# Kernel optimization log

Hardware: AMD Instinct MI355X
Metric: run time of the kernel (lower is better)

The kernel has to match this reference:

```python
import jax, jax.numpy as jnp
import numpy as np

B, T, D, L = 128, 32, 512, 2


def setup_inputs() -> dict:
    key = jax.random.key(0)
    ks = jax.random.split(key, 8)
    s = 0.02
    inp = {
        "cognition_features": jax.random.normal(ks[0], (B, T, D), dtype=jnp.float32),
        # per-layer stacked params (leading dim L)
        "Wq": s * jax.random.normal(ks[1], (L, D, D), dtype=jnp.float32),
        "bq": jnp.zeros((L, D), jnp.float32),
        "Wk": s * jax.random.normal(ks[2], (L, D, D), dtype=jnp.float32),
        "bk": jnp.zeros((L, D), jnp.float32),
        "Wv": s * jax.random.normal(ks[3], (L, D, D), dtype=jnp.float32),
        "bv": jnp.zeros((L, D), jnp.float32),
        "ln1_g": jnp.ones((L, D), jnp.float32),
        "ln1_b": jnp.zeros((L, D), jnp.float32),
        "W1": s * jax.random.normal(ks[4], (L, 4 * D, D), dtype=jnp.float32),
        "b1": jnp.zeros((L, 4 * D), jnp.float32),
        "W2": s * jax.random.normal(ks[5], (L, D, 4 * D), dtype=jnp.float32),
        "b2": jnp.zeros((L, D), jnp.float32),
        "ln2_g": jnp.ones((L, D), jnp.float32),
        "ln2_b": jnp.zeros((L, D), jnp.float32),
        # gate mlp (random instead of zeros/ones init to avoid degenerate constant gate)
        "Ws": s * jax.random.normal(ks[6], (D, 2 * D), dtype=jnp.float32),
        "bs": jnp.zeros((D,), jnp.float32),
    }
    return inp


def _ln(x, g, b, eps=1e-5):
    mu = jnp.mean(x, axis=-1, keepdims=True)
    var = jnp.mean((x - mu) ** 2, axis=-1, keepdims=True)
    return (x - mu) * jax.lax.rsqrt(var + eps) * g + b


def reference(cognition_features, Wq, bq, Wk, bk, Wv, bv, ln1_g, ln1_b,
              W1, b1, W2, b2, ln2_g, ln2_b, Ws, bs):
    b_, t_, d_ = cognition_features.shape
    L_ = Wq.shape[0]
    # memory bank entries are detached originals of earlier batch items
    mem = jax.lax.stop_gradient(cognition_features).reshape(b_ * t_, d_)
    mem_item = jnp.arange(b_ * t_) // t_
    visible = mem_item[None, :] < jnp.arange(b_)[:, None]  # [B, B*T]
    neg = jnp.asarray(-1e9, cognition_features.dtype)
    scale = 1.0 / jnp.sqrt(jnp.asarray(d_, cognition_features.dtype))

    x = cognition_features
    for l in range(L_):
        q = x @ Wq[l].T + bq[l]                      # [B,T,D]
        k = mem @ Wk[l].T + bk[l]                    # [B*T,D]
        v = mem @ Wv[l].T + bv[l]
        s = jnp.einsum('btd,md->btm', q, k) * scale  # [B,T,B*T]
        s = jnp.where(visible[:, None, :], s, neg)
        a = jax.nn.softmax(s, axis=-1)
        attn = jnp.einsum('btm,md->btd', a, v)
        x = _ln(x + attn, ln1_g[l], ln1_b[l])
        h = jax.nn.gelu(x @ W1[l].T + b1[l], approximate=False)
        x = _ln(x + h @ W2[l].T + b2[l], ln2_g[l], ln2_b[l])

    # item 0 has an empty bank: blocks are skipped, attn_out = query
    attn_out = jnp.where((jnp.arange(b_) == 0)[:, None, None], cognition_features, x)
    cat = jnp.concatenate([cognition_features, attn_out], axis=-1)
    g = jax.nn.sigmoid(cat @ Ws.T + bs)
    return g * cognition_features + (1.0 - g) * attn_out
```

## Files before the change

kernel.cpp:

```cpp
#include <hip/hip_runtime.h>
#include <cmath>


#define ROWS 4096
#define DIM  512

typedef __bf16 bf16x8 __attribute__((ext_vector_type(8)));
typedef float  f32x4  __attribute__((ext_vector_type(4)));
typedef unsigned short u16;
typedef u16 u16x4 __attribute__((ext_vector_type(4)));
typedef u16 u16x8 __attribute__((ext_vector_type(8)));

#define RD ((size_t)ROWS * DIM)
#define BUFU 12288

__device__ __forceinline__ u16 f2bf(float x) {
    union { float f; unsigned u; } c; c.f = x;
    const unsigned r = (c.u + 0x7FFFu + ((c.u >> 16) & 1u)) >> 16;
    return (u16)r;
}

__device__ __forceinline__ void gload16(const void* g, void* l) {
    __builtin_amdgcn_global_load_lds(
        (const __attribute__((address_space(1))) void*)g,
        (__attribute__((address_space(3))) void*)l, 16, 0, 0);
}

__device__ __forceinline__ float gelu_f(float v) {
    return 0.5f * v * (1.0f + erff(v * 0.70710678118654752f));
}

template<int EPI>
__device__ __forceinline__ void mgemm_body(
    const u16* __restrict__ A, int lda,
    const u16* __restrict__ B, int ldb,
    const float* __restrict__ bias,
    void* __restrict__ C, int ldc,
    int kBeg, int kEnd, float scale, int m0, int n0, u16* smem)
{
    const int tid  = threadIdx.x;
    const int lane = tid & 63;
    const int w    = tid >> 6;
    const int wr   = (w >> 1) << 5;
    const int wc   = (w & 1) << 6;

    f32x4 acc[2][4];
    #pragma unroll
    for (int i = 0; i < 2; ++i)
        #pragma unroll
        for (int j = 0; j < 4; ++j)
            acc[i][j] = (f32x4){0.f, 0.f, 0.f, 0.f};

    const u16* gpA[2]; int loA[2];
    #pragma unroll
    for (int q = 0; q < 2; ++q) {
        const int c = (q << 2) + w;
        const int s = (c << 6) + lane;
        const int row = s >> 3, sub = (s & 7) ^ (row & 7);
        gpA[q] = A + (size_t)(m0 + row) * lda + (sub << 3) + kBeg;
        loA[q] = c << 9;
    }
    const u16* gpB[4]; int loB[4];
    #pragma unroll
    for (int q = 0; q < 4; ++q) {
        const int c = ((q + 2) << 2) + w - 8;
        const int s = (c << 6) + lane;
        const int row = s >> 3, sub = (s & 7) ^ (row & 7);
        gpB[q] = B + (size_t)(n0 + row) * ldb + (sub << 3) + kBeg;
        loB[q] = 4096 + (c << 9);
    }

    const int l15 = lane & 15, kg = lane >> 4;
    int aoff[2][2], boff[4][2];
    #pragma unroll
    for (int i = 0; i < 2; ++i)
        #pragma unroll
        for (int h = 0; h < 2; ++h) {
            const int r = wr + (i << 4) + l15;
            const int sub = ((h << 2) + kg) ^ (r & 7);
            aoff[i][h] = ((r << 3) + sub) << 3;
        }
    #pragma unroll
    for (int j = 0; j < 4; ++j)
        #pragma unroll
        for (int h = 0; h < 2; ++h) {
            const int r = wc + (j << 4) + l15;
            const int sub = ((h << 2) + kg) ^ (r & 7);
            boff[j][h] = 4096 + (((r << 3) + sub) << 3);
        }

    const int nt = (kEnd - kBeg) >> 6;

    auto STAGE = [&](int t, int bsel) {
        u16* base = smem + bsel * BUFU;
        const int ko = t << 6;
        gload16(gpA[0] + ko, base + loA[0]);
        gload16(gpA[1] + ko, base + loA[1]);
        gload16(gpB[0] + ko, base + loB[0]);
        gload16(gpB[1] + ko, base + loB[1]);
        gload16(gpB[2] + ko, base + loB[2]);
        gload16(gpB[3] + ko, base + loB[3]);
    };

    if (nt > 0) {
        STAGE(0, 0);
        if (nt > 1) STAGE(1, 1);
        for (int t = 0; t < nt; ++t) {
            if (t + 1 < nt) asm volatile("s_waitcnt vmcnt(6)" ::: "memory");
            else            asm volatile("s_waitcnt vmcnt(0)" ::: "memory");
            __builtin_amdgcn_s_barrier();
            asm volatile("" ::: "memory");

            const u16* buf = smem + (t & 1) * BUFU;
            bf16x8 a_[2][2], b_[4][2];
            #pragma unroll
            for (int i = 0; i < 2; ++i)
                #pragma unroll
                for (int h = 0; h < 2; ++h)
                    a_[i][h] = *reinterpret_cast<const bf16x8*>(&buf[aoff[i][h]]);
            #pragma unroll
            for (int j = 0; j < 4; ++j)
                #pragma unroll
                for (int h = 0; h < 2; ++h)
                    b_[j][h] = *reinterpret_cast<const bf16x8*>(&buf[boff[j][h]]);

            asm volatile("s_waitcnt lgkmcnt(0)" ::: "memory");
            __builtin_amdgcn_s_barrier();
            asm volatile("" ::: "memory");

            if (t + 2 < nt) STAGE(t + 2, t & 1);

            __builtin_amdgcn_s_setprio(1);
            #pragma unroll
            for (int h = 0; h < 2; ++h)
                #pragma unroll
                for (int i = 0; i < 2; ++i)
                    #pragma unroll
                    for (int j = 0; j < 4; ++j) {
                        if (EPI == 4)
                            acc[i][j] = __builtin_amdgcn_mfma_f32_16x16x32_bf16(
                                a_[i][h], b_[j][h], acc[i][j], 0, 0, 0);
                        else
                            acc[i][j] = __builtin_amdgcn_mfma_f32_16x16x32_bf16(
                                b_[j][h], a_[i][h], acc[i][j], 0, 0, 0);
                    }
            __builtin_amdgcn_s_setprio(0);
        }
    }

    const int lq = lane >> 4;
    if (EPI == 4) {
        #pragma unroll
        for (int j = 0; j < 4; ++j) {
            const int col = n0 + wc + (j << 4) + l15;
            const float bj = bias[col];
            #pragma unroll
            for (int i = 0; i < 2; ++i) {
                const int row0 = m0 + wr + (i << 4) + (lq << 2);
                u16x4 pk;
                #pragma unroll
                for (int r = 0; r < 4; ++r) pk[r] = f2bf(acc[i][j][r] + bj);
                *reinterpret_cast<u16x4*>(&((u16*)C)[(size_t)col * ldc + row0]) = pk;
            }
        }
    } else {
        #pragma unroll
        for (int j = 0; j < 4; ++j) {
            const int col0 = n0 + wc + (j << 4) + (lq << 2);
            float4 bj = {0.f, 0.f, 0.f, 0.f};
            if (EPI != 0) bj = *reinterpret_cast<const float4*>(&bias[col0]);
            #pragma unroll
            for (int i = 0; i < 2; ++i) {
                const int row = m0 + wr + (i << 4) + l15;
                f32x4 v = acc[i][j];
                if (EPI == 0) {
                    v[0] *= scale; v[1] *= scale; v[2] *= scale; v[3] *= scale;
                    *reinterpret_cast<f32x4*>(&((float*)C)[(size_t)row * ldc + col0]) = v;
                } else if (EPI == 1) {
                    v[0] += bj.x; v[1] += bj.y; v[2] += bj.z; v[3] += bj.w;
                    *reinterpret_cast<f32x4*>(&((float*)C)[(size_t)row * ldc + col0]) = v;
                } else {
                    v[0] += bj.x; v[1] += bj.y; v[2] += bj.z; v[3] += bj.w;
                    if (EPI == 3) {
                        v[0] = gelu_f(v[0]); v[1] = gelu_f(v[1]);
                        v[2] = gelu_f(v[2]); v[3] = gelu_f(v[3]);
                    }
                    u16x4 pk = {f2bf(v[0]), f2bf(v[1]), f2bf(v[2]), f2bf(v[3])};
                    *reinterpret_cast<u16x4*>(&((u16*)C)[(size_t)row * ldc + col0]) = pk;
                }
            }
        }
    }
}

template<int EPI>
__global__ __launch_bounds__(256, 3) void mgemm(
    const u16* __restrict__ A, int lda, const u16* __restrict__ B, int ldb,
    const float* __restrict__ bias, void* __restrict__ C, int ldc, int K, float scale)
{
    const int m0 = blockIdx.x << 6;
    const int n0 = blockIdx.y << 7;
    __shared__ u16 smem[2 * BUFU];
    mgemm_body<EPI>(A, lda, B, ldb, bias, C, ldc, 0, K, scale, m0, n0, smem);
}

__device__ __forceinline__ int tri_pref(int b) {
    const int h = b >> 1;
    return (b & 1) ? (h + 1) * (h + 1) : h * (h + 1);
}
__global__ __launch_bounds__(256, 3) void mgemm_tri(
    const u16* __restrict__ A, const u16* __restrict__ B,
    float* __restrict__ C, float scale)
{
    const int z = blockIdx.x;
    int bx = 2 * (int)sqrtf((float)z);
    while (tri_pref(bx + 1) <= z) ++bx;
    while (tri_pref(bx) > z) --bx;
    const int by = z - tri_pref(bx);
    __shared__ u16 smem[2 * BUFU];
    mgemm_body<0>(A, 512, B, 512, nullptr, C, 4096, 0, 512, scale,
                  bx << 6, by << 7, smem);
}

template<bool AVK>
__global__ __launch_bounds__(256, 3) void mgemm_pk(
    const u16* __restrict__ A, int lda, const u16* __restrict__ B, int ldb,
    float* __restrict__ Cpart, int K, int chunk)
{
    const int m0 = blockIdx.x << 6;
    const int n0 = blockIdx.y << 7;
    const int z  = blockIdx.z;
    const int Klim = AVK ? (m0 + 64) : K;
    const int ch = AVK ? ((((Klim >> 2) + 63) >> 6) << 6) : chunk;
    int kBeg = z * ch; if (kBeg > Klim) kBeg = Klim;
    int kEnd = kBeg + ch; if (kEnd > Klim) kEnd = Klim;
    __shared__ u16 smem[2 * BUFU];
    mgemm_body<0>(A, lda, B, ldb, nullptr, Cpart + (size_t)z * RD, 512,
                  kBeg, kEnd, 1.f, m0, n0, smem);
}

__global__ __launch_bounds__(256, 3) void qkv_gemm(
    const u16* __restrict__ xa, const u16* __restrict__ cfb,
    const u16* __restrict__ Wqb, const u16* __restrict__ Wkb, const u16* __restrict__ Wvb,
    const float* __restrict__ bq, const float* __restrict__ bk, const float* __restrict__ bv,
    u16* __restrict__ q, u16* __restrict__ k, u16* __restrict__ vT)
{
    __shared__ u16 smem[2 * BUFU];
    const int m0 = blockIdx.x << 6;
    const int which = blockIdx.y >> 2;
    const int n0 = (blockIdx.y & 3) << 7;
    if (which == 0)
        mgemm_body<2>(xa,  512, Wqb, 512, bq, q,  512,  0, 512, 1.f, m0, n0, smem);
    else if (which == 1)
        mgemm_body<2>(cfb, 512, Wkb, 512, bk, k,  512,  0, 512, 1.f, m0, n0, smem);
    else
        mgemm_body<4>(cfb, 512, Wvb, 512, bv, vT, 4096, 0, 512, 1.f, m0, n0, smem);
}

__global__ __launch_bounds__(256) void softmax_pbf(
    const float* __restrict__ S, u16* __restrict__ P, float* __restrict__ sums)
{
    const int row = blockIdx.x;
    const int b   = row >> 5;
    const int Lb  = b << 5;
    const int bound = ((row >> 6) + 1) << 6;
    const float* s = S + (size_t)row * 4096;
    u16* p = P + (size_t)row * 4096;
    const int tid = threadIdx.x;

    const u16x8 z8 = {0, 0, 0, 0, 0, 0, 0, 0};
    for (int m = Lb + tid * 8; m < bound; m += 2048)
        *reinterpret_cast<u16x8*>(&p[m]) = z8;
    if (b == 0) { if (tid == 0) sums[row] = 1.f; return; }

    __shared__ float red[4];
    float mx = -3.0e38f;
    for (int m = tid * 4; m < Lb; m += 1024) {
        const float4 v = *reinterpret_cast<const float4*>(&s[m]);
        mx = fmaxf(mx, fmaxf(fmaxf(v.x, v.y), fmaxf(v.z, v.w)));
    }
    #pragma unroll
    for (int off = 32; off; off >>= 1) mx = fmaxf(mx, __shfl_xor(mx, off));
    if ((tid & 63) == 0) red[tid >> 6] = mx;
    __syncthreads();
    mx = fmaxf(fmaxf(red[0], red[1]), fmaxf(red[2], red[3]));
    __syncthreads();

    float sum = 0.f;
    for (int m = tid * 8; m < Lb; m += 2048) {
        const float4 v0 = *reinterpret_cast<const float4*>(&s[m]);
        const float4 v1 = *reinterpret_cast<const float4*>(&s[m + 4]);
        float e[8];
        e[0] = expf(v0.x - mx); e[1] = expf(v0.y - mx);
        e[2] = expf(v0.z - mx); e[3] = expf(v0.w - mx);
        e[4] = expf(v1.x - mx); e[5] = expf(v1.y - mx);
        e[6] = expf(v1.z - mx); e[7] = expf(v1.w - mx);
        u16x8 o;
        #pragma unroll
        for (int i = 0; i < 8; ++i) { sum += e[i]; o[i] = f2bf(e[i]); }
        *reinterpret_cast<u16x8*>(&p[m]) = o;
    }
    #pragma unroll
    for (int off = 32; off; off >>= 1) sum += __shfl_xor(sum, off);
    if ((tid & 63) == 0) red[tid >> 6] = sum;
    __syncthreads();
    if (tid == 0)
        sums[row] = fmaxf(red[0] + red[1] + red[2] + red[3], 1e-30f);
}

template<int NS, bool HASB, bool DIV>
__global__ __launch_bounds__(256) void ln_res_ps(
    const float* __restrict__ Xin, const float* __restrict__ part,
    const float* __restrict__ bias, const float* __restrict__ sums,
    const float* __restrict__ gamma, const float* __restrict__ beta,
    float* __restrict__ Xout, u16* __restrict__ Xbf)
{
    const int row  = blockIdx.x * 4 + (threadIdx.x >> 6);
    const int lane = threadIdx.x & 63;
    const float* xr = Xin + (size_t)row * DIM;
    const int d0 = lane << 3;
    const float inv = DIV ? (1.0f / sums[row]) : 1.0f;

    const float4 x0 = *reinterpret_cast<const float4*>(&xr[d0]);
    const float4 x1 = *reinterpret_cast<const float4*>(&xr[d0 + 4]);
    float a[8] = {0.f, 0.f, 0.f, 0.f, 0.f, 0.f, 0.f, 0.f};
    #pragma unroll
    for (int s = 0; s < NS; ++s) {
        const float* pr = part + (size_t)s * RD + (size_t)row * DIM + d0;
        const float4 p0 = *reinterpret_cast<const float4*>(pr);
        const float4 p1 = *reinterpret_cast<const float4*>(pr + 4);
        a[0] += p0.x; a[1] += p0.y; a[2] += p0.z; a[3] += p0.w;
        a[4] += p1.x; a[5] += p1.y; a[6] += p1.z; a[7] += p1.w;
    }
    float v[8] = {x0.x, x0.y, x0.z, x0.w, x1.x, x1.y, x1.z, x1.w};
    #pragma unroll
    for (int i = 0; i < 8; ++i) v[i] += a[i] * inv;
    if (HASB) {
        const float4 b0 = *reinterpret_cast<const float4*>(&bias[d0]);
        const float4 b1 = *reinterpret_cast<const float4*>(&bias[d0 + 4]);
        v[0] += b0.x; v[1] += b0.y; v[2] += b0.z; v[3] += b0.w;
        v[4] += b1.x; v[5] += b1.y; v[6] += b1.z; v[7] += b1.w;
    }

    float sm = 0.f;
    #pragma unroll
    for (int i = 0; i < 8; ++i) sm += v[i];
    #pragma unroll
    for (int off = 32; off; off >>= 1) sm += __shfl_xor(sm, off);
    const float mu = sm * (1.0f / 512.0f);

    float qs = 0.f;
    #pragma unroll
    for (int i = 0; i < 8; ++i) { const float d = v[i] - mu; qs += d * d; }
    #pragma unroll
    for (int off = 32; off; off >>= 1) qs += __shfl_xor(qs, off);
    const float rs = rsqrtf(qs * (1.0f / 512.0f) + 1e-5f);

    const float4 g0 = *reinterpret_cast<const float4*>(&gamma[d0]);
    const float4 g1 = *reinterpret_cast<const float4*>(&gamma[d0 + 4]);
    const float4 b0 = *reinterpret_cast<const float4*>(&beta[d0]);
    const float4 b1 = *reinterpret_cast<const float4*>(&beta[d0 + 4]);
    float o[8];
    o[0] = (v[0] - mu) * rs * g0.x + b0.x;
    o[1] = (v[1] - mu) * rs * g0.y + b0.y;
    o[2] = (v[2] - mu) * rs * g0.z + b0.z;
    o[3] = (v[3] - mu) * rs * g0.w + b0.w;
    o[4] = (v[4] - mu) * rs * g1.x + b1.x;
    o[5] = (v[5] - mu) * rs * g1.y + b1.y;
    o[6] = (v[6] - mu) * rs * g1.z + b1.z;
    o[7] = (v[7] - mu) * rs * g1.w + b1.w;

    float4 f0 = {o[0], o[1], o[2], o[3]}, f1 = {o[4], o[5], o[6], o[7]};
    *reinterpret_cast<float4*>(&Xout[(size_t)row * DIM + d0])     = f0;
    *reinterpret_cast<float4*>(&Xout[(size_t)row * DIM + d0 + 4]) = f1;
    u16x8 ob;
    #pragma unroll
    for (int i = 0; i < 8; ++i) ob[i] = f2bf(o[i]);
    *reinterpret_cast<u16x8*>(&Xbf[(size_t)row * DIM + d0]) = ob;
}

struct ConvArgs {
    const float* src[7];
    u16* dst[7];
    int start[8];
};

__global__ __launch_bounds__(256) void conv_all(ConvArgs a)
{
    const int b = blockIdx.x;
    int seg = 0;
    #pragma unroll
    for (int i = 1; i < 7; ++i) seg += (a.start[i] <= b) ? 1 : 0;
    const int i = ((b - a.start[seg]) * 256 + threadIdx.x) << 3;
    const float* s = a.src[seg];
    const float4 lo = *reinterpret_cast<const float4*>(&s[i]);
    const float4 hi = *reinterpret_cast<const float4*>(&s[i + 4]);
    u16x8 o = {f2bf(lo.x), f2bf(lo.y), f2bf(lo.z), f2bf(lo.w),
               f2bf(hi.x), f2bf(hi.y), f2bf(hi.z), f2bf(hi.w)};
    *reinterpret_cast<u16x8*>(&a.dst[seg][i]) = o;
}

__global__ __launch_bounds__(256) void build_cat(
    u16* __restrict__ cat, const u16* __restrict__ cfb, const u16* __restrict__ xbf)
{
    const int idx = blockIdx.x * 256 + threadIdx.x;
    const int row = idx >> 7;
    const int c8  = idx & 127;
    const u16* src2 = (row < 32) ? cfb : xbf;
    const u16x8 v = (c8 < 64)
        ? *reinterpret_cast<const u16x8*>(&cfb[(size_t)row * 512 + (c8 << 3)])
        : *reinterpret_cast<const u16x8*>(&src2[(size_t)row * 512 + ((c8 - 64) << 3)]);
    *reinterpret_cast<u16x8*>(&cat[(size_t)row * 1024 + (c8 << 3)]) = v;
}

__global__ __launch_bounds__(256) void final_gate_ps(
    float4* __restrict__ out, const float4* __restrict__ cf,
    const float4* __restrict__ x, const float* __restrict__ part,
    const float* __restrict__ bias)
{
    const int idx = blockIdx.x * 256 + threadIdx.x;
    const int row = idx >> 7;
    const int c4  = idx & 127;
    const float4 zc = cf[idx];
    const float4 p0 = reinterpret_cast<const float4*>(part)[idx];
    const float4 p1 = reinterpret_cast<const float4*>(part + RD)[idx];
    const float4 bb = *reinterpret_cast<const float4*>(&bias[c4 << 2]);
    const float4 za = (row < 32) ? zc : x[idx];
    float4 o;
    { const float g = 1.0f / (1.0f + expf(-(p0.x + p1.x + bb.x))); o.x = g * zc.x + (1.0f - g) * za.x; }
    { const float g = 1.0f / (1.0f + expf(-(p0.y + p1.y + bb.y))); o.y = g * zc.y + (1.0f - g) * za.y; }
    { const float g = 1.0f / (1.0f + expf(-(p0.z + p1.z + bb.z))); o.z = g * zc.z + (1.0f - g) * za.z; }
    { const float g = 1.0f / (1.0f + expf(-(p0.w + p1.w + bb.w))); o.w = g * zc.w + (1.0f - g) * za.w; }
    out[idx] = o;
}

extern "C" void kernel_launch(void* const* d_in, const int* in_sizes, int n_in,
                              void* d_out, int out_size, void* d_ws, size_t ws_size,
                              hipStream_t stream)
{
    const float* cf   = (const float*)d_in[0];
    const float* Wq   = (const float*)d_in[1];
    const float* bq   = (const float*)d_in[2];
    const float* Wk   = (const float*)d_in[3];
    const float* bk   = (const float*)d_in[4];
    const float* Wv   = (const float*)d_in[5];
    const float* bv   = (const float*)d_in[6];
    const float* ln1g = (const float*)d_in[7];
    const float* ln1b = (const float*)d_in[8];
    const float* W1   = (const float*)d_in[9];
    const float* b1   = (const float*)d_in[10];
    const float* W2   = (const float*)d_in[11];
    const float* b2   = (const float*)d_in[12];
    const float* ln2g = (const float*)d_in[13];
    const float* ln2b = (const float*)d_in[14];
    const float* Wsg  = (const float*)d_in[15];
    const float* bsg  = (const float*)d_in[16];
    float* out = (float*)d_out;

    float* ws   = (float*)d_ws;
    float* x    = ws;
    float* sums = ws + RD;
    float* s    = ws + 2 * RD;
    float* part = ws + 2 * RD;
    u16*  pbf  = (u16*)(ws + 10 * RD);
    u16*  hbf  = pbf;
    u16*  catb = pbf;
    u16*  bfb  = (u16*)(ws + 14 * RD);
    u16* cfb = bfb;
    u16* xbf = bfb + RD;
    u16* qbf = bfb + 2 * RD;
    u16* kbf = bfb + 3 * RD;
    u16* vTb = bfb + 4 * RD;
    u16* Wqb = bfb + 5 * RD;
    u16* Wkb = Wqb + 524288;
    u16* Wvb = Wkb + 524288;
    u16* W1b = Wvb + 524288;
    u16* W2b = W1b + 2097152;
    u16* Wsb = W2b + 2097152;

    const float scale = 0.044194173824159216f;

    ConvArgs ca;
    ca.src[0] = cf;  ca.dst[0] = cfb;
    ca.src[1] = Wq;  ca.dst[1] = Wqb;
    ca.src[2] = Wk;  ca.dst[2] = Wkb;
    ca.src[3] = Wv;  ca.dst[3] = Wvb;
    ca.src[4] = W1;  ca.dst[4] = W1b;
    ca.src[5] = W2;  ca.dst[5] = W2b;
    ca.src[6] = Wsg; ca.dst[6] = Wsb;
    ca.start[0] = 0;    ca.start[1] = 1024; ca.start[2] = 1280;
    ca.start[3] = 1536; ca.start[4] = 1792; ca.start[5] = 2816;
    ca.start[6] = 3840; ca.start[7] = 4096;
    conv_all<<<4096, 256, 0, stream>>>(ca);

    for (int l = 0; l < 2; ++l) {
        const u16* xa = (l == 0) ? cfb : xbf;
        qkv_gemm<<<dim3(64, 12), 256, 0, stream>>>(
            xa, cfb, Wqb + l * 262144, Wkb + l * 262144, Wvb + l * 262144,
            bq + l * 512, bk + l * 512, bv + l * 512, qbf, kbf, vTb);
        mgemm_tri<<<1056, 256, 0, stream>>>(qbf, kbf, s, scale);
        softmax_pbf<<<4096, 256, 0, stream>>>(s, pbf, sums);
        mgemm_pk<true><<<dim3(64, 4, 4), 256, 0, stream>>>(
            pbf, 4096, vTb, 4096, part, 4096, 0);
        ln_res_ps<4, false, true><<<1024, 256, 0, stream>>>(
            (l == 0) ? cf : x, part, nullptr, sums,
            ln1g + l * 512, ln1b + l * 512, x, xbf);
        mgemm<3><<<dim3(64, 16), 256, 0, stream>>>(
            xbf, 512, W1b + l * 1048576, 512, b1 + l * 2048, hbf, 2048, 512, 1.f);
        mgemm_pk<false><<<dim3(64, 4, 4), 256, 0, stream>>>(
            hbf, 2048, W2b + l * 1048576, 2048, part, 2048, 512);
        ln_res_ps<4, true, false><<<1024, 256, 0, stream>>>(
            x, part, b2 + l * 512, nullptr,
            ln2g + l * 512, ln2b + l * 512, x, xbf);
    }

    build_cat<<<2048, 256, 0, stream>>>(catb, cfb, xbf);
    mgemm_pk<false><<<dim3(64, 4, 2), 256, 0, stream>>>(
        catb, 1024, Wsb, 1024, part, 1024, 512);
    final_gate_ps<<<2048, 256, 0, stream>>>((float4*)out, (const float4*)cf,
                                            (const float4*)x, part, bsg);
}
```

Measured before the change: 271.2 us.

## Enlarge GEMM tiles to 128x256 with 8-wave blocks and interleaved staged loads

```diff
diff --git a/kernel.cpp b/kernel.cpp
--- a/kernel.cpp
+++ b/kernel.cpp
@@ -12,7 +12,7 @@
 typedef u16 u16x8 __attribute__((ext_vector_type(8)));
 
 #define RD ((size_t)ROWS * DIM)
-#define BUFU 12288
+#define BUFU 24576
 
 __device__ __forceinline__ u16 f2bf(float x) {
     union { float f; unsigned u; } c; c.f = x;
@@ -31,132 +31,164 @@
 }
 
 template<int EPI>
-__device__ __forceinline__ void mgemm_body(
+__device__ __forceinline__ void mg_body(
     const u16* __restrict__ A, int lda,
     const u16* __restrict__ B, int ldb,
     const float* __restrict__ bias,
     void* __restrict__ C, int ldc,
-    int kBeg, int kEnd, float scale, int m0, int n0, u16* smem)
+    int ktBeg, int ktEnd, float scale, int m0, int n0, u16* smem)
 {
     const int tid  = threadIdx.x;
     const int lane = tid & 63;
-    const int w    = tid >> 6;
-    const int wr   = (w >> 1) << 5;
-    const int wc   = (w & 1) << 6;
-
-    f32x4 acc[2][4];
-    #pragma unroll
-    for (int i = 0; i < 2; ++i)
+    const int wid  = tid >> 6;
+    const int wm   = wid >> 2;
+    const int wn   = wid & 3;
+    const int l15  = lane & 15, kg = lane >> 4, lq = lane >> 4;
+
+    f32x4 acc[4][4];
+    #pragma unroll
+    for (int i = 0; i < 4; ++i)
         #pragma unroll
         for (int j = 0; j < 4; ++j)
             acc[i][j] = (f32x4){0.f, 0.f, 0.f, 0.f};
 
-    const u16* gpA[2]; int loA[2];
-    #pragma unroll
-    for (int q = 0; q < 2; ++q) {
-        const int c = (q << 2) + w;
-        const int s = (c << 6) + lane;
-        const int row = s >> 3, sub = (s & 7) ^ (row & 7);
-        gpA[q] = A + (size_t)(m0 + row) * lda + (sub << 3) + kBeg;
-        loA[q] = c << 9;
-    }
-    const u16* gpB[4]; int loB[4];
-    #pragma unroll
-    for (int q = 0; q < 4; ++q) {
-        const int c = ((q + 2) << 2) + w - 8;
-        const int s = (c << 6) + lane;
-        const int row = s >> 3, sub = (s & 7) ^ (row & 7);
-        gpB[q] = B + (size_t)(n0 + row) * ldb + (sub << 3) + kBeg;
-        loB[q] = 4096 + (c << 9);
-    }
-
-    const int l15 = lane & 15, kg = lane >> 4;
-    int aoff[2][2], boff[4][2];
-    #pragma unroll
-    for (int i = 0; i < 2; ++i)
+    const int sA  = tid,        rA  = sA  >> 2, klA  = (sA  & 3) ^ ((rA  >> 1) & 3);
+    const int sB0 = tid,        rB0 = sB0 >> 2, klB0 = (sB0 & 3) ^ ((rB0 >> 1) & 3);
+    const int sB1 = tid + 512,  rB1 = sB1 >> 2, klB1 = (sB1 & 3) ^ ((rB1 >> 1) & 3);
+    const u16* gA  = A + (size_t)(m0 + rA)  * lda + (klA  << 3) + (size_t)ktBeg * 64;
+    const u16* gB0 = B + (size_t)(n0 + rB0) * ldb + (klB0 << 3) + (size_t)ktBeg * 64;
+    const u16* gB1 = B + (size_t)(n0 + rB1) * ldb + (klB1 << 3) + (size_t)ktBeg * 64;
+    const int dA0 = sA << 3;
+    const int dB0a = 4096  + (sB0 << 3), dB0b = 4096  + (sB1 << 3);
+    const int dA1 = 12288 + (sA << 3);
+    const int dB1a = 16384 + (sB0 << 3), dB1b = 16384 + (sB1 << 3);
+
+    int aoff[2][4], boff[2][4];
+    #pragma unroll
+    for (int ks = 0; ks < 2; ++ks) {
         #pragma unroll
-        for (int h = 0; h < 2; ++h) {
-            const int r = wr + (i << 4) + l15;
-            const int sub = ((h << 2) + kg) ^ (r & 7);
-            aoff[i][h] = ((r << 3) + sub) << 3;
+        for (int ri = 0; ri < 4; ++ri) {
+            const int r = wm * 64 + ri * 16 + l15;
+            aoff[ks][ri] = (ks ? 12288 : 0) + ((r << 2) + (kg ^ ((r >> 1) & 3)) << 3);
         }
-    #pragma unroll
-    for (int j = 0; j < 4; ++j)
         #pragma unroll
-        for (int h = 0; h < 2; ++h) {
-            const int r = wc + (j << 4) + l15;
-            const int sub = ((h << 2) + kg) ^ (r & 7);
-            boff[j][h] = 4096 + (((r << 3) + sub) << 3);
+        for (int cj = 0; cj < 4; ++cj) {
+            const int r = wn * 64 + cj * 16 + l15;
+            boff[ks][cj] = (ks ? 16384 : 4096) + ((r << 2) + (kg ^ ((r >> 1) & 3)) << 3);
         }
-
-    const int nt = (kEnd - kBeg) >> 6;
-
-    auto STAGE = [&](int t, int bsel) {
-        u16* base = smem + bsel * BUFU;
-        const int ko = t << 6;
-        gload16(gpA[0] + ko, base + loA[0]);
-        gload16(gpA[1] + ko, base + loA[1]);
-        gload16(gpB[0] + ko, base + loB[0]);
-        gload16(gpB[1] + ko, base + loB[1]);
-        gload16(gpB[2] + ko, base + loB[2]);
-        gload16(gpB[3] + ko, base + loB[3]);
-    };
+    }
+
+    const int nt = ktEnd - ktBeg;
 
     if (nt > 0) {
-        STAGE(0, 0);
-        if (nt > 1) STAGE(1, 1);
+        {
+            u16* bb = smem;
+            gload16(gA,       bb + dA0);
+            gload16(gB0,      bb + dB0a);
+            gload16(gB1,      bb + dB0b);
+            gload16(gA + 32,  bb + dA1);
+            gload16(gB0 + 32, bb + dB1a);
+            gload16(gB1 + 32, bb + dB1b);
+        }
         for (int t = 0; t < nt; ++t) {
-            if (t + 1 < nt) asm volatile("s_waitcnt vmcnt(6)" ::: "memory");
-            else            asm volatile("s_waitcnt vmcnt(0)" ::: "memory");
+            const u16* bc = smem + (t & 1) * BUFU;
+            u16* bn = smem + ((t + 1) & 1) * BUFU;
+            const bool more = (t + 1 < nt);
+            const int ko = (t + 1) << 6;
+
+            bf16x8 a0, a1, b_[4];
+
+            asm volatile("s_waitcnt vmcnt(3)" ::: "memory");
             __builtin_amdgcn_s_barrier();
             asm volatile("" ::: "memory");
-
-            const u16* buf = smem + (t & 1) * BUFU;
-            bf16x8 a_[2][2], b_[4][2];
-            #pragma unroll
-            for (int i = 0; i < 2; ++i)
-                #pragma unroll
-                for (int h = 0; h < 2; ++h)
-                    a_[i][h] = *reinterpret_cast<const bf16x8*>(&buf[aoff[i][h]]);
+            a0 = *reinterpret_cast<const bf16x8*>(&bc[aoff[0][0]]);
+            a1 = *reinterpret_cast<const bf16x8*>(&bc[aoff[0][1]]);
             #pragma unroll
             for (int j = 0; j < 4; ++j)
-                #pragma unroll
-                for (int h = 0; h < 2; ++h)
-                    b_[j][h] = *reinterpret_cast<const bf16x8*>(&buf[boff[j][h]]);
-
-            asm volatile("s_waitcnt lgkmcnt(0)" ::: "memory");
+                b_[j] = *reinterpret_cast<const bf16x8*>(&bc[boff[0][j]]);
+            if (more) gload16(gA + ko, bn + dA0);
+            __builtin_amdgcn_s_setprio(1);
+            #pragma unroll
+            for (int j = 0; j < 4; ++j) {
+                if (EPI == 4) {
+                    acc[0][j] = __builtin_amdgcn_mfma_f32_16x16x32_bf16(a0, b_[j], acc[0][j], 0, 0, 0);
+                    acc[1][j] = __builtin_amdgcn_mfma_f32_16x16x32_bf16(a1, b_[j], acc[1][j], 0, 0, 0);
+                } else {
+                    acc[0][j] = __builtin_amdgcn_mfma_f32_16x16x32_bf16(b_[j], a0, acc[0][j], 0, 0, 0);
+                    acc[1][j] = __builtin_amdgcn_mfma_f32_16x16x32_bf16(b_[j], a1, acc[1][j], 0, 0, 0);
+                }
+            }
+            __builtin_amdgcn_s_setprio(0);
+
             __builtin_amdgcn_s_barrier();
             asm volatile("" ::: "memory");
-
-            if (t + 2 < nt) STAGE(t + 2, t & 1);
-
+            a0 = *reinterpret_cast<const bf16x8*>(&bc[aoff[0][2]]);
+            a1 = *reinterpret_cast<const bf16x8*>(&bc[aoff[0][3]]);
+            if (more) { gload16(gB0 + ko, bn + dB0a); gload16(gB1 + ko, bn + dB0b); }
             __builtin_amdgcn_s_setprio(1);
             #pragma unroll
-            for (int h = 0; h < 2; ++h)
-                #pragma unroll
-                for (int i = 0; i < 2; ++i)
-                    #pragma unroll
-                    for (int j = 0; j < 4; ++j) {
-                        if (EPI == 4)
-                            acc[i][j] = __builtin_amdgcn_mfma_f32_16x16x32_bf16(
-                                a_[i][h], b_[j][h], acc[i][j], 0, 0, 0);
-                        else
-                            acc[i][j] = __builtin_amdgcn_mfma_f32_16x16x32_bf16(
-                                b_[j][h], a_[i][h], acc[i][j], 0, 0, 0);
-                    }
+            for (int j = 0; j < 4; ++j) {
+                if (EPI == 4) {
+                    acc[2][j] = __builtin_amdgcn_mfma_f32_16x16x32_bf16(a0, b_[j], acc[2][j], 0, 0, 0);
+                    acc[3][j] = __builtin_amdgcn_mfma_f32_16x16x32_bf16(a1, b_[j], acc[3][j], 0, 0, 0);
+                } else {
+                    acc[2][j] = __builtin_amdgcn_mfma_f32_16x16x32_bf16(b_[j], a0, acc[2][j], 0, 0, 0);
+                    acc[3][j] = __builtin_amdgcn_mfma_f32_16x16x32_bf16(b_[j], a1, acc[3][j], 0, 0, 0);
+                }
+            }
+            __builtin_amdgcn_s_setprio(0);
+
+            if (more) asm volatile("s_waitcnt vmcnt(3)" ::: "memory");
+            else      asm volatile("s_waitcnt vmcnt(0)" ::: "memory");
+            __builtin_amdgcn_s_barrier();
+            asm volatile("" ::: "memory");
+            a0 = *reinterpret_cast<const bf16x8*>(&bc[aoff[1][0]]);
+            a1 = *reinterpret_cast<const bf16x8*>(&bc[aoff[1][1]]);
+            #pragma unroll
+            for (int j = 0; j < 4; ++j)
+                b_[j] = *reinterpret_cast<const bf16x8*>(&bc[boff[1][j]]);
+            if (more) gload16(gA + ko + 32, bn + dA1);
+            __builtin_amdgcn_s_setprio(1);
+            #pragma unroll
+            for (int j = 0; j < 4; ++j) {
+                if (EPI == 4) {
+                    acc[0][j] = __builtin_amdgcn_mfma_f32_16x16x32_bf16(a0, b_[j], acc[0][j], 0, 0, 0);
+                    acc[1][j] = __builtin_amdgcn_mfma_f32_16x16x32_bf16(a1, b_[j], acc[1][j], 0, 0, 0);
+                } else {
+                    acc[0][j] = __builtin_amdgcn_mfma_f32_16x16x32_bf16(b_[j], a0, acc[0][j], 0, 0, 0);
+                    acc[1][j] = __builtin_amdgcn_mfma_f32_16x16x32_bf16(b_[j], a1, acc[1][j], 0, 0, 0);
+                }
+            }
+            __builtin_amdgcn_s_setprio(0);
+
+            __builtin_amdgcn_s_barrier();
+            asm volatile("" ::: "memory");
+            a0 = *reinterpret_cast<const bf16x8*>(&bc[aoff[1][2]]);
+            a1 = *reinterpret_cast<const bf16x8*>(&bc[aoff[1][3]]);
+            if (more) { gload16(gB0 + ko + 32, bn + dB1a); gload16(gB1 + ko + 32, bn + dB1b); }
+            __builtin_amdgcn_s_setprio(1);
+            #pragma unroll
+            for (int j = 0; j < 4; ++j) {
+                if (EPI == 4) {
+                    acc[2][j] = __builtin_amdgcn_mfma_f32_16x16x32_bf16(a0, b_[j], acc[2][j], 0, 0, 0);
+                    acc[3][j] = __builtin_amdgcn_mfma_f32_16x16x32_bf16(a1, b_[j], acc[3][j], 0, 0, 0);
+                } else {
+                    acc[2][j] = __builtin_amdgcn_mfma_f32_16x16x32_bf16(b_[j], a0, acc[2][j], 0, 0, 0);
+                    acc[3][j] = __builtin_amdgcn_mfma_f32_16x16x32_bf16(b_[j], a1, acc[3][j], 0, 0, 0);
+                }
+            }
             __builtin_amdgcn_s_setprio(0);
         }
     }
 
-    const int lq = lane >> 4;
     if (EPI == 4) {
         #pragma unroll
         for (int j = 0; j < 4; ++j) {
-            const int col = n0 + wc + (j << 4) + l15;
+            const int col = n0 + wn * 64 + (j << 4) + l15;
             const float bj = bias[col];
             #pragma unroll
-            for (int i = 0; i < 2; ++i) {
-                const int row0 = m0 + wr + (i << 4) + (lq << 2);
+            for (int i = 0; i < 4; ++i) {
+                const int row0 = m0 + wm * 64 + (i << 4) + (lq << 2);
                 u16x4 pk;
                 #pragma unroll
                 for (int r = 0; r < 4; ++r) pk[r] = f2bf(acc[i][j][r] + bj);
@@ -166,18 +198,15 @@
     } else {
         #pragma unroll
         for (int j = 0; j < 4; ++j) {
-            const int col0 = n0 + wc + (j << 4) + (lq << 2);
+            const int col0 = n0 + wn * 64 + (j << 4) + (lq << 2);
             float4 bj = {0.f, 0.f, 0.f, 0.f};
             if (EPI != 0) bj = *reinterpret_cast<const float4*>(&bias[col0]);
             #pragma unroll
-            for (int i = 0; i < 2; ++i) {
-                const int row = m0 + wr + (i << 4) + l15;
+            for (int i = 0; i < 4; ++i) {
+                const int row = m0 + wm * 64 + (i << 4) + l15;
                 f32x4 v = acc[i][j];
                 if (EPI == 0) {
                     v[0] *= scale; v[1] *= scale; v[2] *= scale; v[3] *= scale;
-                    *reinterpret_cast<f32x4*>(&((float*)C)[(size_t)row * ldc + col0]) = v;
-                } else if (EPI == 1) {
-                    v[0] += bj.x; v[1] += bj.y; v[2] += bj.z; v[3] += bj.w;
                     *reinterpret_cast<f32x4*>(&((float*)C)[(size_t)row * ldc + col0]) = v;
                 } else {
                     v[0] += bj.x; v[1] += bj.y; v[2] += bj.z; v[3] += bj.w;
@@ -193,68 +222,84 @@
     }
 }
 
-template<int EPI>
-__global__ __launch_bounds__(256, 3) void mgemm(
-    const u16* __restrict__ A, int lda, const u16* __restrict__ B, int ldb,
-    const float* __restrict__ bias, void* __restrict__ C, int ldc, int K, float scale)
-{
-    const int m0 = blockIdx.x << 6;
-    const int n0 = blockIdx.y << 7;
+__global__ __launch_bounds__(512, 2) void g_qkv(
+    const u16* __restrict__ xa, const u16* __restrict__ cfb,
+    const u16* __restrict__ Wqb, const u16* __restrict__ Wkb,
+    const u16* __restrict__ Wvb,
+    const float* __restrict__ bq, const float* __restrict__ bk,
+    const float* __restrict__ bv,
+    u16* __restrict__ q, u16* __restrict__ k, u16* __restrict__ vT)
+{
     __shared__ u16 smem[2 * BUFU];
-    mgemm_body<EPI>(A, lda, B, ldb, bias, C, ldc, 0, K, scale, m0, n0, smem);
+    const int m0 = blockIdx.x << 7;
+    const int which = blockIdx.y >> 1;
+    const int n0 = (blockIdx.y & 1) << 8;
+    if (which == 0)
+        mg_body<2>(xa,  512, Wqb, 512, bq, q,  512,  0, 8, 1.f, m0, n0, smem);
+    else if (which == 1)
+        mg_body<2>(cfb, 512, Wkb, 512, bk, k,  512,  0, 8, 1.f, m0, n0, smem);
+    else
+        mg_body<4>(cfb, 512, Wvb, 512, bv, vT, 4096, 0, 8, 1.f, m0, n0, smem);
 }
 
 __device__ __forceinline__ int tri_pref(int b) {
     const int h = b >> 1;
     return (b & 1) ? (h + 1) * (h + 1) : h * (h + 1);
 }
-__global__ __launch_bounds__(256, 3) void mgemm_tri(
-    const u16* __restrict__ A, const u16* __restrict__ B,
-    float* __restrict__ C, float scale)
+__global__ __launch_bounds__(512, 2) void g_tri(
+    const u16* __restrict__ qb, const u16* __restrict__ kb,
+    float* __restrict__ S, float scale)
 {
     const int z = blockIdx.x;
-    int bx = 2 * (int)sqrtf((float)z);
-    while (tri_pref(bx + 1) <= z) ++bx;
-    while (tri_pref(bx) > z) --bx;
-    const int by = z - tri_pref(bx);
+    int mt = 2 * (int)sqrtf((float)z);
+    while (tri_pref(mt + 1) <= z) ++mt;
+    while (tri_pref(mt) > z) --mt;
+    const int nt = z - tri_pref(mt);
     __shared__ u16 smem[2 * BUFU];
-    mgemm_body<0>(A, 512, B, 512, nullptr, C, 4096, 0, 512, scale,
-                  bx << 6, by << 7, smem);
-}
-
-template<bool AVK>
-__global__ __launch_bounds__(256, 3) void mgemm_pk(
-    const u16* __restrict__ A, int lda, const u16* __restrict__ B, int ldb,
-    float* __restrict__ Cpart, int K, int chunk)
-{
-    const int m0 = blockIdx.x << 6;
-    const int n0 = blockIdx.y << 7;
-    const int z  = blockIdx.z;
-    const int Klim = AVK ? (m0 + 64) : K;
-    const int ch = AVK ? ((((Klim >> 2) + 63) >> 6) << 6) : chunk;
-    int kBeg = z * ch; if (kBeg > Klim) kBeg = Klim;
-    int kEnd = kBeg + ch; if (kEnd > Klim) kEnd = Klim;
+    mg_body<0>(qb, 512, kb, 512, nullptr, S, 4096, 0, 8, scale, mt << 7, nt << 8, smem);
+}
+
+__global__ __launch_bounds__(512, 2) void g_av(
+    const u16* __restrict__ P, const u16* __restrict__ vT,
+    float* __restrict__ part)
+{
+    const int mt = blockIdx.x, n0 = blockIdx.y << 8, z = blockIdx.z;
+    const int kts = 2 * mt + 2;
+    const int ch = (kts + 3) >> 2;
+    int kb = z * ch; if (kb > kts) kb = kts;
+    int ke = kb + ch; if (ke > kts) ke = kts;
     __shared__ u16 smem[2 * BUFU];
-    mgemm_body<0>(A, lda, B, ldb, nullptr, Cpart + (size_t)z * RD, 512,
-                  kBeg, kEnd, 1.f, m0, n0, smem);
-}
-
-__global__ __launch_bounds__(256, 3) void qkv_gemm(
-    const u16* __restrict__ xa, const u16* __restrict__ cfb,
-    const u16* __restrict__ Wqb, const u16* __restrict__ Wkb, const u16* __restrict__ Wvb,
-    const float* __restrict__ bq, const float* __restrict__ bk, const float* __restrict__ bv,
-    u16* __restrict__ q, u16* __restrict__ k, u16* __restrict__ vT)
+    mg_body<0>(P, 4096, vT, 4096, nullptr, part + (size_t)z * RD, 512,
+               kb, ke, 1.f, mt << 7, n0, smem);
+}
+
+__global__ __launch_bounds__(512, 2) void g_mlp1(
+    const u16* __restrict__ xb, const u16* __restrict__ W1b,
+    const float* __restrict__ b1, u16* __restrict__ h)
 {
     __shared__ u16 smem[2 * BUFU];
-    const int m0 = blockIdx.x << 6;
-    const int which = blockIdx.y >> 2;
-    const int n0 = (blockIdx.y & 3) << 7;
-    if (which == 0)
-        mgemm_body<2>(xa,  512, Wqb, 512, bq, q,  512,  0, 512, 1.f, m0, n0, smem);
-    else if (which == 1)
-        mgemm_body<2>(cfb, 512, Wkb, 512, bk, k,  512,  0, 512, 1.f, m0, n0, smem);
-    else
-        mgemm_body<4>(cfb, 512, Wvb, 512, bv, vT, 4096, 0, 512, 1.f, m0, n0, smem);
+    mg_body<3>(xb, 512, W1b, 512, b1, h, 2048, 0, 8, 1.f,
+               blockIdx.x << 7, blockIdx.y << 8, smem);
+}
+
+__global__ __launch_bounds__(512, 2) void g_mlp2(
+    const u16* __restrict__ h, const u16* __restrict__ W2b,
+    float* __restrict__ part)
+{
+    const int z = blockIdx.z;
+    __shared__ u16 smem[2 * BUFU];
+    mg_body<0>(h, 2048, W2b, 2048, nullptr, part + (size_t)z * RD, 512,
+               z * 8, z * 8 + 8, 1.f, blockIdx.x << 7, blockIdx.y << 8, smem);
+}
+
+__global__ __launch_bounds__(512, 2) void g_gate(
+    const u16* __restrict__ cat, const u16* __restrict__ Wsb,
+    float* __restrict__ part)
+{
+    const int z = blockIdx.z;
+    __shared__ u16 smem[2 * BUFU];
+    mg_body<0>(cat, 1024, Wsb, 1024, nullptr, part + (size_t)z * RD, 512,
+               z * 8, z * 8 + 8, 1.f, blockIdx.x << 7, blockIdx.y << 8, smem);
 }
 
 __global__ __launch_bounds__(256) void softmax_pbf(
@@ -263,7 +308,7 @@
     const int row = blockIdx.x;
     const int b   = row >> 5;
     const int Lb  = b << 5;
-    const int bound = ((row >> 6) + 1) << 6;
+    const int bound = ((row >> 7) + 1) << 7;
     const float* s = S + (size_t)row * 4096;
     u16* p = P + (size_t)row * 4096;
     const int tid = threadIdx.x;
@@ -463,8 +508,8 @@
     float* s    = ws + 2 * RD;
     float* part = ws + 2 * RD;
     u16*  pbf  = (u16*)(ws + 10 * RD);
-    u16*  hbf  = pbf;
-    u16*  catb = pbf;
+    u16*  hbf  = (u16*)(ws + 10 * RD);
+    u16*  catb = (u16*)(ws + 10 * RD);
     u16*  bfb  = (u16*)(ws + 14 * RD);
     u16* cfb = bfb;
     u16* xbf = bfb + RD;
@@ -495,28 +540,25 @@
 
     for (int l = 0; l < 2; ++l) {
         const u16* xa = (l == 0) ? cfb : xbf;
-        qkv_gemm<<<dim3(64, 12), 256, 0, stream>>>(
+        g_qkv<<<dim3(32, 6), 512, 0, stream>>>(
             xa, cfb, Wqb + l * 262144, Wkb + l * 262144, Wvb + l * 262144,
             bq + l * 512, bk + l * 512, bv + l * 512, qbf, kbf, vTb);
-        mgemm_tri<<<1056, 256, 0, stream>>>(qbf, kbf, s, scale);
+        g_tri<<<272, 512, 0, stream>>>(qbf, kbf, s, scale);
         softmax_pbf<<<4096, 256, 0, stream>>>(s, pbf, sums);
-        mgemm_pk<true><<<dim3(64, 4, 4), 256, 0, stream>>>(
-            pbf, 4096, vTb, 4096, part, 4096, 0);
+        g_av<<<dim3(32, 2, 4), 512, 0, stream>>>(pbf, vTb, part);
         ln_res_ps<4, false, true><<<1024, 256, 0, stream>>>(
             (l == 0) ? cf : x, part, nullptr, sums,
             ln1g + l * 512, ln1b + l * 512, x, xbf);
-        mgemm<3><<<dim3(64, 16), 256, 0, stream>>>(
-            xbf, 512, W1b + l * 1048576, 512, b1 + l * 2048, hbf, 2048, 512, 1.f);
-        mgemm_pk<false><<<dim3(64, 4, 4), 256, 0, stream>>>(
-            hbf, 2048, W2b + l * 1048576, 2048, part, 2048, 512);
+        g_mlp1<<<dim3(32, 8), 512, 0, stream>>>(
+            xbf, W1b + l * 1048576, b1 + l * 2048, hbf);
+        g_mlp2<<<dim3(32, 2, 4), 512, 0, stream>>>(hbf, W2b + l * 1048576, part);
         ln_res_ps<4, true, false><<<1024, 256, 0, stream>>>(
             x, part, b2 + l * 512, nullptr,
             ln2g + l * 512, ln2b + l * 512, x, xbf);
     }
 
     build_cat<<<2048, 256, 0, stream>>>(catb, cfb, xbf);
-    mgemm_pk<false><<<dim3(64, 4, 2), 256, 0, stream>>>(
-        catb, 1024, Wsb, 1024, part, 1024, 512);
+    g_gate<<<dim3(32, 2, 2), 512, 0, stream>>>(catb, Wsb, part);
     final_gate_ps<<<2048, 256, 0, stream>>>((float4*)out, (const float4*)cf,
                                             (const float4*)x, part, bsg);
 }
```

After: 307.8 us. 13.5% more time.

## Fuse softmax exponentiation into the QK^T GEMM epilogue and drop the concat copy

Applied to the files above, without the earlier changes.

```diff
diff --git a/kernel.cpp b/kernel.cpp
--- a/kernel.cpp
+++ b/kernel.cpp
@@ -36,7 +36,8 @@
     const u16* __restrict__ B, int ldb,
     const float* __restrict__ bias,
     void* __restrict__ C, int ldc,
-    int kBeg, int kEnd, float scale, int m0, int n0, u16* smem)
+    int kBeg, int kEnd, float scale, int m0, int n0, u16* smem,
+    float* __restrict__ sums)
 {
     const int tid  = threadIdx.x;
     const int lane = tid & 63;
@@ -162,6 +163,34 @@
                 for (int r = 0; r < 4; ++r) pk[r] = f2bf(acc[i][j][r] + bj);
                 *reinterpret_cast<u16x4*>(&((u16*)C)[(size_t)col * ldc + row0]) = pk;
             }
+        }
+    } else if (EPI == 5) {
+        float rs0 = 0.f, rs1 = 0.f;
+        #pragma unroll
+        for (int j = 0; j < 4; ++j) {
+            const int col0 = n0 + wc + (j << 4) + (lq << 2);
+            #pragma unroll
+            for (int i = 0; i < 2; ++i) {
+                const int row = m0 + wr + (i << 4) + l15;
+                const int lim = (row >> 5) << 5;
+                f32x4 v = acc[i][j];
+                u16x4 pk;
+                float rsl = 0.f;
+                #pragma unroll
+                for (int r = 0; r < 4; ++r) {
+                    const float e = (col0 + r < lim) ? __expf(v[r] * scale) : 0.f;
+                    rsl += e;
+                    pk[r] = f2bf(e);
+                }
+                if (i == 0) rs0 += rsl; else rs1 += rsl;
+                *reinterpret_cast<u16x4*>(&((u16*)C)[(size_t)row * ldc + col0]) = pk;
+            }
+        }
+        rs0 += __shfl_xor(rs0, 16); rs0 += __shfl_xor(rs0, 32);
+        rs1 += __shfl_xor(rs1, 16); rs1 += __shfl_xor(rs1, 32);
+        if (lq == 0) {
+            atomicAdd(&sums[m0 + wr + l15], rs0);
+            atomicAdd(&sums[m0 + wr + 16 + l15], rs1);
         }
     } else {
         #pragma unroll
@@ -201,7 +230,7 @@
     const int m0 = blockIdx.x << 6;
     const int n0 = blockIdx.y << 7;
     __shared__ u16 smem[2 * BUFU];
-    mgemm_body<EPI>(A, lda, B, ldb, bias, C, ldc, 0, K, scale, m0, n0, smem);
+    mgemm_body<EPI>(A, lda, B, ldb, bias, C, ldc, 0, K, scale, m0, n0, smem, nullptr);
 }
 
 __device__ __forceinline__ int tri_pref(int b) {
@@ -210,7 +239,7 @@
 }
 __global__ __launch_bounds__(256, 3) void mgemm_tri(
     const u16* __restrict__ A, const u16* __restrict__ B,
-    float* __restrict__ C, float scale)
+    u16* __restrict__ P, float* __restrict__ sums, float scale)
 {
     const int z = blockIdx.x;
     int bx = 2 * (int)sqrtf((float)z);
@@ -218,8 +247,8 @@
     while (tri_pref(bx) > z) --bx;
     const int by = z - tri_pref(bx);
     __shared__ u16 smem[2 * BUFU];
-    mgemm_body<0>(A, 512, B, 512, nullptr, C, 4096, 0, 512, scale,
-                  bx << 6, by << 7, smem);
+    mgemm_body<5>(A, 512, B, 512, nullptr, P, 4096, 0, 512, scale,
+                  bx << 6, by << 7, smem, sums);
 }
 
 template<bool AVK>
@@ -236,7 +265,18 @@
     int kEnd = kBeg + ch; if (kEnd > Klim) kEnd = Klim;
     __shared__ u16 smem[2 * BUFU];
     mgemm_body<0>(A, lda, B, ldb, nullptr, Cpart + (size_t)z * RD, 512,
-                  kBeg, kEnd, 1.f, m0, n0, smem);
+                  kBeg, kEnd, 1.f, m0, n0, smem, nullptr);
+}
+
+__global__ __launch_bounds__(256, 3) void mgemm_part(
+    const u16* __restrict__ A, int lda, const u16* __restrict__ B, int ldb,
+    float* __restrict__ Cpart)
+{
+    const int m0 = blockIdx.x << 6;
+    const int n0 = blockIdx.y << 7;
+    __shared__ u16 smem[2 * BUFU];
+    mgemm_body<0>(A, lda, B, ldb, nullptr, Cpart, 512,
+                  0, 512, 1.f, m0, n0, smem, nullptr);
 }
 
 __global__ __launch_bounds__(256, 3) void qkv_gemm(
@@ -250,62 +290,11 @@
     const int which = blockIdx.y >> 2;
     const int n0 = (blockIdx.y & 3) << 7;
     if (which == 0)
-        mgemm_body<2>(xa,  512, Wqb, 512, bq, q,  512,  0, 512, 1.f, m0, n0, smem);
+        mgemm_body<2>(xa,  512, Wqb, 512, bq, q,  512,  0, 512, 1.f, m0, n0, smem, nullptr);
     else if (which == 1)
-        mgemm_body<2>(cfb, 512, Wkb, 512, bk, k,  512,  0, 512, 1.f, m0, n0, smem);
+        mgemm_body<2>(cfb, 512, Wkb, 512, bk, k,  512,  0, 512, 1.f, m0, n0, smem, nullptr);
     else
-        mgemm_body<4>(cfb, 512, Wvb, 512, bv, vT, 4096, 0, 512, 1.f, m0, n0, smem);
-}
-
-__global__ __launch_bounds__(256) void softmax_pbf(
-    const float* __restrict__ S, u16* __restrict__ P, float* __restrict__ sums)
-{
-    const int row = blockIdx.x;
-    const int b   = row >> 5;
-    const int Lb  = b << 5;
-    const int bound = ((row >> 6) + 1) << 6;
-    const float* s = S + (size_t)row * 4096;
-    u16* p = P + (size_t)row * 4096;
-    const int tid = threadIdx.x;
-
-    const u16x8 z8 = {0, 0, 0, 0, 0, 0, 0, 0};
-    for (int m = Lb + tid * 8; m < bound; m += 2048)
-        *reinterpret_cast<u16x8*>(&p[m]) = z8;
-    if (b == 0) { if (tid == 0) sums[row] = 1.f; return; }
-
-    __shared__ float red[4];
-    float mx = -3.0e38f;
-    for (int m = tid * 4; m < Lb; m += 1024) {
-        const float4 v = *reinterpret_cast<const float4*>(&s[m]);
-        mx = fmaxf(mx, fmaxf(fmaxf(v.x, v.y), fmaxf(v.z, v.w)));
-    }
-    #pragma unroll
-    for (int off = 32; off; off >>= 1) mx = fmaxf(mx, __shfl_xor(mx, off));
-    if ((tid & 63) == 0) red[tid >> 6] = mx;
-    __syncthreads();
-    mx = fmaxf(fmaxf(red[0], red[1]), fmaxf(red[2], red[3]));
-    __syncthreads();
-
-    float sum = 0.f;
-    for (int m = tid * 8; m < Lb; m += 2048) {
-        const float4 v0 = *reinterpret_cast<const float4*>(&s[m]);
-        const float4 v1 = *reinterpret_cast<const float4*>(&s[m + 4]);
-        float e[8];
-        e[0] = expf(v0.x - mx); e[1] = expf(v0.y - mx);
-        e[2] = expf(v0.z - mx); e[3] = expf(v0.w - mx);
-        e[4] = expf(v1.x - mx); e[5] = expf(v1.y - mx);
-        e[6] = expf(v1.z - mx); e[7] = expf(v1.w - mx);
-        u16x8 o;
-        #pragma unroll
-        for (int i = 0; i < 8; ++i) { sum += e[i]; o[i] = f2bf(e[i]); }
-        *reinterpret_cast<u16x8*>(&p[m]) = o;
-    }
-    #pragma unroll
-    for (int off = 32; off; off >>= 1) sum += __shfl_xor(sum, off);
-    if ((tid & 63) == 0) red[tid >> 6] = sum;
-    __syncthreads();
-    if (tid == 0)
-        sums[row] = fmaxf(red[0] + red[1] + red[2] + red[3], 1e-30f);
+        mgemm_body<4>(cfb, 512, Wvb, 512, bv, vT, 4096, 0, 512, 1.f, m0, n0, smem, nullptr);
 }
 
 template<int NS, bool HASB, bool DIV>
@@ -319,7 +308,7 @@
     const int lane = threadIdx.x & 63;
     const float* xr = Xin + (size_t)row * DIM;
     const int d0 = lane << 3;
-    const float inv = DIV ? (1.0f / sums[row]) : 1.0f;
+    const float inv = DIV ? (1.0f / fmaxf(sums[row], 1e-30f)) : 1.0f;
 
     const float4 x0 = *reinterpret_cast<const float4*>(&xr[d0]);
     const float4 x1 = *reinterpret_cast<const float4*>(&xr[d0 + 4]);
@@ -400,17 +389,17 @@
     *reinterpret_cast<u16x8*>(&a.dst[seg][i]) = o;
 }
 
-__global__ __launch_bounds__(256) void build_cat(
-    u16* __restrict__ cat, const u16* __restrict__ cfb, const u16* __restrict__ xbf)
-{
-    const int idx = blockIdx.x * 256 + threadIdx.x;
-    const int row = idx >> 7;
-    const int c8  = idx & 127;
-    const u16* src2 = (row < 32) ? cfb : xbf;
-    const u16x8 v = (c8 < 64)
-        ? *reinterpret_cast<const u16x8*>(&cfb[(size_t)row * 512 + (c8 << 3)])
-        : *reinterpret_cast<const u16x8*>(&src2[(size_t)row * 512 + ((c8 - 64) << 3)]);
-    *reinterpret_cast<u16x8*>(&cat[(size_t)row * 1024 + (c8 << 3)]) = v;
+__global__ __launch_bounds__(256) void zero_sums(float4* __restrict__ s)
+{
+    s[blockIdx.x * 256 + threadIdx.x] = (float4){0.f, 0.f, 0.f, 0.f};
+}
+
+__global__ __launch_bounds__(256) void fix_x0(u16* __restrict__ xbf,
+                                              const u16* __restrict__ cfb)
+{
+    const int i = (blockIdx.x * 256 + threadIdx.x) << 3;
+    *reinterpret_cast<u16x8*>(&xbf[i]) =
+        *reinterpret_cast<const u16x8*>(&cfb[i]);
 }
 
 __global__ __launch_bounds__(256) void final_gate_ps(
@@ -460,11 +449,9 @@
     float* ws   = (float*)d_ws;
     float* x    = ws;
     float* sums = ws + RD;
-    float* s    = ws + 2 * RD;
     float* part = ws + 2 * RD;
     u16*  pbf  = (u16*)(ws + 10 * RD);
-    u16*  hbf  = pbf;
-    u16*  catb = pbf;
+    u16*  hbf  = (u16*)(ws + 10 * RD);
     u16*  bfb  = (u16*)(ws + 14 * RD);
     u16* cfb = bfb;
     u16* xbf = bfb + RD;
@@ -495,11 +482,11 @@
 
     for (int l = 0; l < 2; ++l) {
         const u16* xa = (l == 0) ? cfb : xbf;
+        zero_sums<<<4, 256, 0, stream>>>((float4*)sums);
         qkv_gemm<<<dim3(64, 12), 256, 0, stream>>>(
             xa, cfb, Wqb + l * 262144, Wkb + l * 262144, Wvb + l * 262144,
             bq + l * 512, bk + l * 512, bv + l * 512, qbf, kbf, vTb);
-        mgemm_tri<<<1056, 256, 0, stream>>>(qbf, kbf, s, scale);
-        softmax_pbf<<<4096, 256, 0, stream>>>(s, pbf, sums);
+        mgemm_tri<<<1056, 256, 0, stream>>>(qbf, kbf, pbf, sums, scale);
         mgemm_pk<true><<<dim3(64, 4, 4), 256, 0, stream>>>(
             pbf, 4096, vTb, 4096, part, 4096, 0);
         ln_res_ps<4, false, true><<<1024, 256, 0, stream>>>(
@@ -514,9 +501,9 @@
             ln2g + l * 512, ln2b + l * 512, x, xbf);
     }
 
-    build_cat<<<2048, 256, 0, stream>>>(catb, cfb, xbf);
-    mgemm_pk<false><<<dim3(64, 4, 2), 256, 0, stream>>>(
-        catb, 1024, Wsb, 1024, part, 1024, 512);
+    fix_x0<<<8, 256, 0, stream>>>(xbf, cfb);
+    mgemm_part<<<dim3(64, 4), 256, 0, stream>>>(cfb, 512, Wsb,       1024, part);
+    mgemm_part<<<dim3(64, 4), 256, 0, stream>>>(xbf, 512, Wsb + 512, 1024, part + RD);
     final_gate_ps<<<2048, 256, 0, stream>>>((float4*)out, (const float4*)cf,
                                             (const float4*)x, part, bsg);
 }
```

Result: faster. 251.5 us (-7.3%).
